# Kernel optimization log

Hardware: AMD Instinct MI355X
Metric: run time of the kernel (lower is better)

Reference implementation:

```python
import jax, jax.numpy as jnp
import numpy as np

jax.config.update("jax_enable_x64", True)

N_QUBITS = 21
N_LAYERS = 2
N_PARAMS = (N_LAYERS + 1) * N_QUBITS  # 63

# CNOT in |ctrl,tgt> basis, reshaped to (c_out, t_out, c_in, t_in)
_CNOT = jnp.array([[1, 0, 0, 0],
                   [0, 1, 0, 0],
                   [0, 0, 0, 1],
                   [0, 0, 1, 0]], dtype=jnp.complex128).reshape(2, 2, 2, 2)


def _ry(theta):
    # RY(theta) = [[cos(t/2), -sin(t/2)], [sin(t/2), cos(t/2)]]
    c = jnp.cos(theta * 0.5).astype(jnp.complex128)
    s = jnp.sin(theta * 0.5).astype(jnp.complex128)
    return jnp.stack([jnp.stack([c, -s]), jnp.stack([s, c])])


def _apply_1q(state, gate, q):
    # Contract 2x2 gate into qubit axis q of the (2,)*n state tensor.
    state = jnp.tensordot(gate, state, axes=((1,), (q,)))
    return jnp.moveaxis(state, 0, q)


def _apply_cnot(state, q):
    # CNOT with control q, target q+1 (qubit 0 = most-significant axis).
    state = jnp.tensordot(_CNOT, state, axes=((2, 3), (q, q + 1)))
    return jnp.moveaxis(state, (0, 1), (q, q + 1))


def setup_inputs() -> dict:
    key = jax.random.key(0)
    params = jax.random.uniform(key, (N_PARAMS,), dtype=jnp.float32) * (2.0 * np.pi)
    return {"params": params}


def reference(params):
    p = params.astype(jnp.float64)
    # |0...0> as a (2,)*n tensor
    state = jnp.zeros((2,) * N_QUBITS, dtype=jnp.complex128)
    state = state.at[(0,) * N_QUBITS].set(1.0 + 0.0j)
    idx = 0
    for _ in range(N_LAYERS):
        for q in range(N_QUBITS):
            state = _apply_1q(state, _ry(p[idx]), q)
            idx += 1
        for q in range(N_QUBITS - 1):
            state = _apply_cnot(state, q)
    for q in range(N_QUBITS):
        state = _apply_1q(state, _ry(p[idx]), q)
        idx += 1
    state = state.reshape(-1)  # (2**N_QUBITS,)
    return state / jnp.linalg.norm(state)
```

## Files before the change

### kernel.cpp

```cpp
#include <hip/hip_runtime.h>


#define NQ 21
#define NSTATE (1 << NQ)
#define SW(t) ((t) + ((t) >> 5))

typedef float f32x4 __attribute__((ext_vector_type(4)));

template <int BIT, int N>
__device__ __forceinline__ void ry_bf(float (&v)[N], float c, float s) {
#pragma unroll
  for (int m = 0; m < N; ++m)
    if ((m & (1 << BIT)) == 0) {
      float a = v[m], b = v[m | (1 << BIT)];
      v[m] = c * a - s * b;
      v[m | (1 << BIT)] = s * a + c * b;
    }
}

template <int CBIT, int TBIT, int N>
__device__ __forceinline__ void cnot_rr(float (&v)[N]) {
#pragma unroll
  for (int m = 0; m < N; ++m)
    if ((m & (1 << CBIT)) && !(m & (1 << TBIT))) {
      float t = v[m];
      v[m] = v[m | (1 << TBIT)];
      v[m | (1 << TBIT)] = t;
    }
}

__global__ __launch_bounds__(512, 4) void fused(const float* __restrict__ p,
                                                float* __restrict__ out,
                                                int outmode) {
  __shared__ float2 csn[63];
  __shared__ float ex[2][8448];
  const int tid = threadIdx.x;
  const int bid = blockIdx.x;
  if (tid < 63) {
    float h = 0.5f * p[tid];
    csn[tid] = float2{__cosf(h) * 0.0f + cosf(h), sinf(h)};
  }
  __syncthreads();

  float W[2][2];
  {
    const int b0 = (bid >> 7) & 1;
    const float2 g30 = csn[42], g20 = csn[21], g10 = csn[0];
    const float r00 = b0 ? g30.y : g30.x;
    const float r01 = b0 ? g30.x : -g30.y;
    float w00 = r00 * g20.x * g10.x;
    float w01 = r00 * (-g20.y) * g10.y;
    float w10 = r01 * g20.y * g10.x;
    float w11 = r01 * g20.x * g10.y;
#pragma unroll
    for (int q = 1; q <= 7; ++q) {
      const int bq = (bid >> (7 - q)) & 1;
      const float2 g1 = csn[q], g2 = csn[21 + q], g3 = csn[42 + q];
      const float c1 = g1.x, s1 = g1.y;
      const float c2 = g2.x, s2 = g2.y;
      const float c3 = g3.x, s3 = g3.y;
      const float h00 = c1 * w00 + s1 * w01;
      const float h01 = c1 * w10 + s1 * w11;
      const float h10 = s1 * w00 + c1 * w01;
      const float h11 = s1 * w10 + c1 * w11;
      const float m00 = c2 * h00 + s2 * h01;
      const float m01 = s2 * h00 + c2 * h01;
      const float m10 = -s2 * h10 + c2 * h11;
      const float m11 = c2 * h10 - s2 * h11;
      const float r0 = bq ? s3 : c3;
      const float r1 = bq ? c3 : -s3;
      w00 = r0 * m00;
      w01 = r0 * m10;
      w10 = r1 * m01;
      w11 = r1 * m11;
    }
    const float2 g18 = csn[8], g28 = csn[29], g9 = csn[9];
    const float hh00 = g18.x * w00 + g18.y * w01;
    const float hh01 = g18.x * w10 + g18.y * w11;
    const float hh10 = g18.y * w00 + g18.x * w01;
    const float hh11 = g18.y * w10 + g18.x * w11;
    const float a00 = g28.x * hh00 + g28.y * hh01;
    const float a10 = g28.y * hh00 + g28.x * hh01;
    const float a01 = -g28.y * hh10 + g28.x * hh11;
    const float a11 = g28.x * hh10 - g28.y * hh11;
    W[0][0] = a00 * g9.x + a01 * g9.y;
    W[0][1] = a00 * g9.y + a01 * g9.x;
    W[1][0] = a10 * g9.x + a11 * g9.y;
    W[1][1] = a10 * g9.y + a11 * g9.x;
  }

  float v[16];
  {
    const int gt = tid ^ (tid >> 1);
    float tcommon = 1.0f;
#pragma unroll
    for (int b = 0; b < 8; ++b) {
      const float2 gb = csn[20 - b];
      tcommon *= ((gt >> b) & 1) ? gb.y : gb.x;
    }
    const float2 g12 = csn[12], g11 = csn[11], g10 = csn[10];
    const int t8 = (tid >> 8) & 1;
    const float s12_0 = t8 ? g12.y : g12.x;
    const float s12_1 = t8 ? g12.x : g12.y;
#pragma unroll
    for (int r = 0; r < 16; ++r) {
      const int gr = r ^ (r >> 1);
      float prod = tcommon * W[(r >> 3) & 1][(r >> 2) & 1];
      prod *= (r & 1) ? s12_1 : s12_0;
      prod *= (gr & 1) ? g11.y : g11.x;
      prod *= ((gr >> 1) & 1) ? g10.y : g10.x;
      v[r] = prod;
    }
  }

  ry_bf<2>(v, csn[30].x, csn[30].y);
  ry_bf<1>(v, csn[31].x, csn[31].y);
  ry_bf<0>(v, csn[32].x, csn[32].y);
  cnot_rr<3, 2>(v);
  cnot_rr<2, 1>(v);
  cnot_rr<1, 0>(v);
  ry_bf<3>(v, csn[50].x, csn[50].y);
  ry_bf<2>(v, csn[51].x, csn[51].y);
  ry_bf<1>(v, csn[52].x, csn[52].y);

#pragma unroll
  for (int r = 0; r < 16; ++r) ex[0][SW((r << 9) | tid)] = v[r];
  __syncthreads();
#pragma unroll
  for (int r = 0; r < 16; ++r)
    v[r] = ex[0][SW(((tid >> 6) << 10) | (r << 6) | (tid & 63))];

  ry_bf<2>(v, csn[33].x, csn[33].y);
  ry_bf<1>(v, csn[34].x, csn[34].y);
  ry_bf<0>(v, csn[35].x, csn[35].y);
  cnot_rr<3, 2>(v);
  cnot_rr<2, 1>(v);
  cnot_rr<1, 0>(v);
  ry_bf<3>(v, csn[53].x, csn[53].y);
  ry_bf<2>(v, csn[54].x, csn[54].y);
  ry_bf<1>(v, csn[55].x, csn[55].y);

#pragma unroll
  for (int r = 0; r < 16; ++r)
    ex[1][SW(((tid >> 6) << 10) | (r << 6) | (tid & 63))] = v[r];
  __syncthreads();
#pragma unroll
  for (int r = 0; r < 16; ++r)
    v[r] = ex[1][SW(((tid >> 3) << 7) | (r << 3) | (tid & 7))];

  ry_bf<2>(v, csn[36].x, csn[36].y);
  ry_bf<1>(v, csn[37].x, csn[37].y);
  ry_bf<0>(v, csn[38].x, csn[38].y);
  cnot_rr<3, 2>(v);
  cnot_rr<2, 1>(v);
  cnot_rr<1, 0>(v);
  ry_bf<3>(v, csn[56].x, csn[56].y);
  ry_bf<2>(v, csn[57].x, csn[57].y);
  ry_bf<1>(v, csn[58].x, csn[58].y);

#pragma unroll
  for (int r = 0; r < 16; ++r)
    ex[0][SW(((tid >> 3) << 7) | (r << 3) | (tid & 7))] = v[r];
  __syncthreads();
#pragma unroll
  for (int r = 0; r < 16; ++r) v[r] = ex[0][SW((tid << 4) | r)];

  ry_bf<2>(v, csn[39].x, csn[39].y);
  ry_bf<1>(v, csn[40].x, csn[40].y);
  ry_bf<0>(v, csn[41].x, csn[41].y);
  cnot_rr<3, 2>(v);
  cnot_rr<2, 1>(v);
  cnot_rr<1, 0>(v);
  ry_bf<3>(v, csn[59].x, csn[59].y);
  ry_bf<2>(v, csn[60].x, csn[60].y);
  ry_bf<1>(v, csn[61].x, csn[61].y);
  ry_bf<0>(v, csn[62].x, csn[62].y);

  const int base = (bid << 13) | (tid << 4);
  if (outmode == 2) {
    f32x4* o4 = (f32x4*)out;
#pragma unroll
    for (int i = 0; i < 8; ++i) {
      f32x4 w = {v[2 * i], 0.0f, v[2 * i + 1], 0.0f};
      __builtin_nontemporal_store(w, &o4[(base >> 1) + i]);
    }
  } else {
    f32x4* o4 = (f32x4*)(out + base);
#pragma unroll
    for (int j = 0; j < 4; ++j) {
      f32x4 w = {v[4 * j], v[4 * j + 1], v[4 * j + 2], v[4 * j + 3]};
      __builtin_nontemporal_store(w, &o4[j]);
    }
  }
}

extern "C" void kernel_launch(void* const* d_in, const int* in_sizes, int n_in,
                              void* d_out, int out_size, void* d_ws,
                              size_t ws_size, hipStream_t stream) {
  const float* p = (const float*)d_in[0];
  float* out = (float*)d_out;
  const int outmode = (out_size == 2 * NSTATE) ? 2 : 1;
  fused<<<256, 512, 0, stream>>>(p, out, outmode);
}
```

Before: 61.81 us.

## Repartition state into 1024 blocks of 256 threads with 8 amplitudes each

Changes the decomposition from 256 blocks × 512 threads × 16 amplitudes to 1024 blocks × 256 threads × 8 amplitudes. Two more qubits are folded into the per-block analytic prefix, and the in-block stage shrinks to 11 qubits, handled with four shared-memory exchange rounds instead of three. The goal is more blocks across the CUs, smaller per-block shared memory and fewer registers per thread. In exchange there are more barriers and shared-memory passes, and the per-block setup and trig work is repeated across four times as many blocks.

```diff
diff --git a/kernel.cpp b/kernel.cpp
--- a/kernel.cpp
+++ b/kernel.cpp
@@ -29,22 +29,22 @@
     }
 }
 
-__global__ __launch_bounds__(512, 4) void fused(const float* __restrict__ p,
+__global__ __launch_bounds__(256, 4) void fused(const float* __restrict__ p,
                                                 float* __restrict__ out,
                                                 int outmode) {
   __shared__ float2 csn[63];
-  __shared__ float ex[2][8448];
+  __shared__ float ex[2][2112];
   const int tid = threadIdx.x;
   const int bid = blockIdx.x;
   if (tid < 63) {
     float h = 0.5f * p[tid];
-    csn[tid] = float2{__cosf(h) * 0.0f + cosf(h), sinf(h)};
+    csn[tid] = float2{cosf(h), sinf(h)};
   }
   __syncthreads();
 
   float W[2][2];
   {
-    const int b0 = (bid >> 7) & 1;
+    const int b0 = (bid >> 9) & 1;
     const float2 g30 = csn[42], g20 = csn[21], g10 = csn[0];
     const float r00 = b0 ? g30.y : g30.x;
     const float r01 = b0 ? g30.x : -g30.y;
@@ -53,8 +53,8 @@
     float w10 = r01 * g20.y * g10.x;
     float w11 = r01 * g20.x * g10.y;
 #pragma unroll
-    for (int q = 1; q <= 7; ++q) {
-      const int bq = (bid >> (7 - q)) & 1;
+    for (int q = 1; q <= 9; ++q) {
+      const int bq = (bid >> (9 - q)) & 1;
       const float2 g1 = csn[q], g2 = csn[21 + q], g3 = csn[42 + q];
       const float c1 = g1.x, s1 = g1.y;
       const float c2 = g2.x, s2 = g2.y;
@@ -74,120 +74,122 @@
       w10 = r1 * m01;
       w11 = r1 * m11;
     }
-    const float2 g18 = csn[8], g28 = csn[29], g9 = csn[9];
-    const float hh00 = g18.x * w00 + g18.y * w01;
-    const float hh01 = g18.x * w10 + g18.y * w11;
-    const float hh10 = g18.y * w00 + g18.x * w01;
-    const float hh11 = g18.y * w10 + g18.x * w11;
-    const float a00 = g28.x * hh00 + g28.y * hh01;
-    const float a10 = g28.y * hh00 + g28.x * hh01;
-    const float a01 = -g28.y * hh10 + g28.x * hh11;
-    const float a11 = g28.x * hh10 - g28.y * hh11;
-    W[0][0] = a00 * g9.x + a01 * g9.y;
-    W[0][1] = a00 * g9.y + a01 * g9.x;
-    W[1][0] = a10 * g9.x + a11 * g9.y;
-    W[1][1] = a10 * g9.y + a11 * g9.x;
-  }
-
-  float v[16];
+    const float2 g1b = csn[10], g2b = csn[31], gW = csn[11];
+    const float hh00 = g1b.x * w00 + g1b.y * w01;
+    const float hh01 = g1b.x * w10 + g1b.y * w11;
+    const float hh10 = g1b.y * w00 + g1b.x * w01;
+    const float hh11 = g1b.y * w10 + g1b.x * w11;
+    const float a00 = g2b.x * hh00 + g2b.y * hh01;
+    const float a10 = g2b.y * hh00 + g2b.x * hh01;
+    const float a01 = -g2b.y * hh10 + g2b.x * hh11;
+    const float a11 = g2b.x * hh10 - g2b.y * hh11;
+    W[0][0] = a00 * gW.x + a01 * gW.y;
+    W[0][1] = a00 * gW.y + a01 * gW.x;
+    W[1][0] = a10 * gW.x + a11 * gW.y;
+    W[1][1] = a10 * gW.y + a11 * gW.x;
+  }
+
+  float v[8];
   {
     const int gt = tid ^ (tid >> 1);
     float tcommon = 1.0f;
 #pragma unroll
-    for (int b = 0; b < 8; ++b) {
+    for (int b = 0; b < 7; ++b) {
       const float2 gb = csn[20 - b];
       tcommon *= ((gt >> b) & 1) ? gb.y : gb.x;
     }
-    const float2 g12 = csn[12], g11 = csn[11], g10 = csn[10];
-    const int t8 = (tid >> 8) & 1;
-    const float s12_0 = t8 ? g12.y : g12.x;
-    const float s12_1 = t8 ? g12.x : g12.y;
-#pragma unroll
-    for (int r = 0; r < 16; ++r) {
+    const int t7 = (tid >> 7) & 1;
+    const float2 g13 = csn[13], g12 = csn[12];
+    const float s13_0 = t7 ? g13.y : g13.x;
+    const float s13_1 = t7 ? g13.x : g13.y;
+#pragma unroll
+    for (int r = 0; r < 8; ++r) {
       const int gr = r ^ (r >> 1);
-      float prod = tcommon * W[(r >> 3) & 1][(r >> 2) & 1];
-      prod *= (r & 1) ? s12_1 : s12_0;
-      prod *= (gr & 1) ? g11.y : g11.x;
-      prod *= ((gr >> 1) & 1) ? g10.y : g10.x;
+      float prod = tcommon * W[(r >> 2) & 1][(r >> 1) & 1];
+      prod *= (r & 1) ? s13_1 : s13_0;
+      prod *= (gr & 1) ? g12.y : g12.x;
       v[r] = prod;
     }
   }
 
-  ry_bf<2>(v, csn[30].x, csn[30].y);
-  ry_bf<1>(v, csn[31].x, csn[31].y);
-  ry_bf<0>(v, csn[32].x, csn[32].y);
-  cnot_rr<3, 2>(v);
-  cnot_rr<2, 1>(v);
-  cnot_rr<1, 0>(v);
-  ry_bf<3>(v, csn[50].x, csn[50].y);
-  ry_bf<2>(v, csn[51].x, csn[51].y);
-  ry_bf<1>(v, csn[52].x, csn[52].y);
-
-#pragma unroll
-  for (int r = 0; r < 16; ++r) ex[0][SW((r << 9) | tid)] = v[r];
-  __syncthreads();
-#pragma unroll
-  for (int r = 0; r < 16; ++r)
-    v[r] = ex[0][SW(((tid >> 6) << 10) | (r << 6) | (tid & 63))];
-
-  ry_bf<2>(v, csn[33].x, csn[33].y);
+  ry_bf<1>(v, csn[32].x, csn[32].y);
+  ry_bf<0>(v, csn[33].x, csn[33].y);
+  cnot_rr<2, 1>(v);
+  cnot_rr<1, 0>(v);
+  ry_bf<2>(v, csn[52].x, csn[52].y);
+  ry_bf<1>(v, csn[53].x, csn[53].y);
+
+#pragma unroll
+  for (int r = 0; r < 8; ++r) ex[0][SW((r << 8) | tid)] = v[r];
+  __syncthreads();
+#pragma unroll
+  for (int r = 0; r < 8; ++r)
+    v[r] = ex[0][SW(((tid >> 6) << 9) | (r << 6) | (tid & 63))];
+
   ry_bf<1>(v, csn[34].x, csn[34].y);
   ry_bf<0>(v, csn[35].x, csn[35].y);
-  cnot_rr<3, 2>(v);
-  cnot_rr<2, 1>(v);
-  cnot_rr<1, 0>(v);
-  ry_bf<3>(v, csn[53].x, csn[53].y);
+  cnot_rr<2, 1>(v);
+  cnot_rr<1, 0>(v);
   ry_bf<2>(v, csn[54].x, csn[54].y);
   ry_bf<1>(v, csn[55].x, csn[55].y);
 
 #pragma unroll
-  for (int r = 0; r < 16; ++r)
-    ex[1][SW(((tid >> 6) << 10) | (r << 6) | (tid & 63))] = v[r];
-  __syncthreads();
-#pragma unroll
-  for (int r = 0; r < 16; ++r)
-    v[r] = ex[1][SW(((tid >> 3) << 7) | (r << 3) | (tid & 7))];
-
-  ry_bf<2>(v, csn[36].x, csn[36].y);
-  ry_bf<1>(v, csn[37].x, csn[37].y);
-  ry_bf<0>(v, csn[38].x, csn[38].y);
-  cnot_rr<3, 2>(v);
-  cnot_rr<2, 1>(v);
-  cnot_rr<1, 0>(v);
-  ry_bf<3>(v, csn[56].x, csn[56].y);
-  ry_bf<2>(v, csn[57].x, csn[57].y);
-  ry_bf<1>(v, csn[58].x, csn[58].y);
-
-#pragma unroll
-  for (int r = 0; r < 16; ++r)
-    ex[0][SW(((tid >> 3) << 7) | (r << 3) | (tid & 7))] = v[r];
-  __syncthreads();
-#pragma unroll
-  for (int r = 0; r < 16; ++r) v[r] = ex[0][SW((tid << 4) | r)];
-
-  ry_bf<2>(v, csn[39].x, csn[39].y);
+  for (int r = 0; r < 8; ++r)
+    ex[1][SW(((tid >> 6) << 9) | (r << 6) | (tid & 63))] = v[r];
+  __syncthreads();
+#pragma unroll
+  for (int r = 0; r < 8; ++r)
+    v[r] = ex[1][SW(((tid >> 4) << 7) | (r << 4) | (tid & 15))];
+
+  ry_bf<1>(v, csn[36].x, csn[36].y);
+  ry_bf<0>(v, csn[37].x, csn[37].y);
+  cnot_rr<2, 1>(v);
+  cnot_rr<1, 0>(v);
+  ry_bf<2>(v, csn[56].x, csn[56].y);
+  ry_bf<1>(v, csn[57].x, csn[57].y);
+
+#pragma unroll
+  for (int r = 0; r < 8; ++r)
+    ex[0][SW(((tid >> 4) << 7) | (r << 4) | (tid & 15))] = v[r];
+  __syncthreads();
+#pragma unroll
+  for (int r = 0; r < 8; ++r)
+    v[r] = ex[0][SW(((tid >> 2) << 5) | (r << 2) | (tid & 3))];
+
+  ry_bf<1>(v, csn[38].x, csn[38].y);
+  ry_bf<0>(v, csn[39].x, csn[39].y);
+  cnot_rr<2, 1>(v);
+  cnot_rr<1, 0>(v);
+  ry_bf<2>(v, csn[58].x, csn[58].y);
+  ry_bf<1>(v, csn[59].x, csn[59].y);
+
+#pragma unroll
+  for (int r = 0; r < 8; ++r)
+    ex[1][SW(((tid >> 2) << 5) | (r << 2) | (tid & 3))] = v[r];
+  __syncthreads();
+#pragma unroll
+  for (int r = 0; r < 8; ++r) v[r] = ex[1][SW((tid << 3) | r)];
+
   ry_bf<1>(v, csn[40].x, csn[40].y);
   ry_bf<0>(v, csn[41].x, csn[41].y);
-  cnot_rr<3, 2>(v);
-  cnot_rr<2, 1>(v);
-  cnot_rr<1, 0>(v);
-  ry_bf<3>(v, csn[59].x, csn[59].y);
+  cnot_rr<2, 1>(v);
+  cnot_rr<1, 0>(v);
   ry_bf<2>(v, csn[60].x, csn[60].y);
   ry_bf<1>(v, csn[61].x, csn[61].y);
   ry_bf<0>(v, csn[62].x, csn[62].y);
 
-  const int base = (bid << 13) | (tid << 4);
+  const int base = (bid << 11) | (tid << 3);
   if (outmode == 2) {
     f32x4* o4 = (f32x4*)out;
 #pragma unroll
-    for (int i = 0; i < 8; ++i) {
+    for (int i = 0; i < 4; ++i) {
       f32x4 w = {v[2 * i], 0.0f, v[2 * i + 1], 0.0f};
       __builtin_nontemporal_store(w, &o4[(base >> 1) + i]);
     }
   } else {
     f32x4* o4 = (f32x4*)(out + base);
 #pragma unroll
-    for (int j = 0; j < 4; ++j) {
+    for (int j = 0; j < 2; ++j) {
       f32x4 w = {v[4 * j], v[4 * j + 1], v[4 * j + 2], v[4 * j + 3]};
       __builtin_nontemporal_store(w, &o4[j]);
     }
@@ -200,5 +202,5 @@
   const float* p = (const float*)d_in[0];
   float* out = (float*)d_out;
   const int outmode = (out_size == 2 * NSTATE) ? 2 : 1;
-  fused<<<256, 512, 0, stream>>>(p, out, outmode);
-}
+  fused<<<1024, 256, 0, stream>>>(p, out, outmode);
+}
```

Result: faster. 59.88 us (-3.1%).
